# Kernel tuning notes

Hardware: AMD Instinct MI355X
Metric: run time of the kernel (lower is better)

## Reference

```python
import jax, jax.numpy as jnp
import numpy as np

N1, N2, N3 = 40000, 30000, 30000
N = N1 + N2 + N3          # total nodes after vstack
E = 800000                # edges
D_IN = 256                # in_channels
D_HID = 256               # 2 * out_channels
D_OUT = 128               # out_channels


def _glorot(k, shape):
    lim = (6.0 / (shape[0] + shape[1])) ** 0.5
    return jax.random.uniform(k, shape, jnp.float32, -lim, lim)


def setup_inputs() -> dict:
    key = jax.random.key(0)
    ks = jax.random.split(key, 12)
    x1 = jax.random.normal(ks[0], (N1, 128), jnp.float32)
    x2 = jax.random.normal(ks[1], (N2, 256), jnp.float32)
    x3 = jax.random.normal(ks[2], (N3, 64), jnp.float32)
    edge_index = jax.random.randint(ks[3], (2, E), 0, N, jnp.int64)
    return {
        "x1": x1, "x2": x2, "x3": x3,
        "Wp1": _glorot(ks[4], (128, D_IN)), "bp1": jnp.zeros((D_IN,), jnp.float32),
        "Wp2": _glorot(ks[5], (256, D_IN)), "bp2": jnp.zeros((D_IN,), jnp.float32),
        "Wp3": _glorot(ks[6], (64, D_IN)),  "bp3": jnp.zeros((D_IN,), jnp.float32),
        "W1": _glorot(ks[7], (D_IN, D_HID)), "b1": jnp.zeros((D_HID,), jnp.float32),
        "W2": _glorot(ks[8], (D_HID, D_OUT)), "b2": jnp.zeros((D_OUT,), jnp.float32),
        "edge_index": edge_index,
    }


def _gcn_conv(x, W, b, src, dst, dis):
    # PyG GCNConv: h = xW; out[j] = sum_i norm_ij * h[i] (incl. self-loop) + b
    h = x @ W                                   # [N, d_out]
    msg = h[src] * (dis[src] * dis[dst])[:, None]   # [E, d_out] edge messages
    agg = jax.ops.segment_sum(msg, dst, num_segments=N)
    agg = agg + h * (dis * dis)[:, None]        # self-loop term (norm = 1/deg)
    return agg + b


def reference(x1, x2, x3, Wp1, bp1, Wp2, bp2, Wp3, bp3, W1, b1, W2, b2, edge_index):
    # per-type projection + vstack
    x = jnp.concatenate([x1 @ Wp1 + bp1, x2 @ Wp2 + bp2, x3 @ Wp3 + bp3], axis=0)
    # dropout(p=0.5) is identity in eval mode (deterministic baseline)
    src, dst = edge_index[0], edge_index[1]
    # degree with self-loops (in-degree at dst, as in PyG gcn_norm)
    deg = jnp.ones((N,), x.dtype).at[dst].add(1.0)
    dis = jax.lax.rsqrt(deg)                    # deg^{-1/2}
    h = jax.nn.relu(_gcn_conv(x, W1, b1, src, dst, dis))
    return _gcn_conv(h, W2, b2, src, dst, dis)
```

## Files before the change

kernel.cpp:

```cpp
#include <hip/hip_runtime.h>
#include <cstddef>

#define NT 100000
#define NN1 40000
#define NN2 30000
#define NN3 30000
#define EE 800000
#define DIN 256
#define DHID 256
#define DOUT 128

typedef _Float16 f16;
typedef f16 f16x8 __attribute__((ext_vector_type(8)));
typedef f16 f16x4 __attribute__((ext_vector_type(4)));
typedef f16 f16x2 __attribute__((ext_vector_type(2)));
typedef float f32x4 __attribute__((ext_vector_type(4)));

static inline int cdiv(int a, int b) { return (a + b - 1) / b; }

__device__ __forceinline__ void gload_lds16(const f16* g, f16* l) {
    __builtin_amdgcn_global_load_lds(
        (const __attribute__((address_space(1))) void*)g,
        (__attribute__((address_space(3))) void*)l, 16, 0, 0);
}

__global__ void k_hist(const int* __restrict__ dst, int* __restrict__ cnt, int e) {
    int i = blockIdx.x * blockDim.x + threadIdx.x;
    if (i < e) atomicAdd(&cnt[dst[i]], 1);
}

__global__ void k_scan1(const int* __restrict__ cnt, int* __restrict__ rowptr,
                        int* __restrict__ part, float* __restrict__ dis, int n) {
    __shared__ int sums[256];
    int b = blockIdx.x, t = threadIdx.x;
    int base = b * 1024 + t * 4;
    int v0 = (base + 0 < n) ? cnt[base + 0] : 0;
    int v1 = (base + 1 < n) ? cnt[base + 1] : 0;
    int v2 = (base + 2 < n) ? cnt[base + 2] : 0;
    int v3 = (base + 3 < n) ? cnt[base + 3] : 0;
    if (base + 0 < n) dis[base + 0] = rsqrtf((float)v0 + 1.0f);
    if (base + 1 < n) dis[base + 1] = rsqrtf((float)v1 + 1.0f);
    if (base + 2 < n) dis[base + 2] = rsqrtf((float)v2 + 1.0f);
    if (base + 3 < n) dis[base + 3] = rsqrtf((float)v3 + 1.0f);
    int tsum = v0 + v1 + v2 + v3;
    sums[t] = tsum;
    __syncthreads();
    for (int off = 1; off < 256; off <<= 1) {
        int y = (t >= off) ? sums[t - off] : 0;
        __syncthreads();
        sums[t] += y;
        __syncthreads();
    }
    int excl = sums[t] - tsum;
    if (base + 0 < n) rowptr[base + 0] = excl;
    if (base + 1 < n) rowptr[base + 1] = excl + v0;
    if (base + 2 < n) rowptr[base + 2] = excl + v0 + v1;
    if (base + 3 < n) rowptr[base + 3] = excl + v0 + v1 + v2;
    if (t == 255) part[b] = sums[255];
}

__global__ void k_scan2(int* __restrict__ part, int nb) {
    __shared__ int sums[256];
    int t = threadIdx.x;
    int v = (t < nb) ? part[t] : 0;
    sums[t] = v;
    __syncthreads();
    for (int off = 1; off < 256; off <<= 1) {
        int y = (t >= off) ? sums[t - off] : 0;
        __syncthreads();
        sums[t] += y;
        __syncthreads();
    }
    if (t < nb) part[t] = sums[t] - v;
}

__global__ void k_scan3(int* __restrict__ rowptr, const int* __restrict__ part,
                        int n, int total) {
    int i = blockIdx.x * blockDim.x + threadIdx.x;
    if (i < n) rowptr[i] += part[i >> 10];
    if (i == 0) rowptr[n] = total;
}

__global__ void k_fill(const int* __restrict__ src, const int* __restrict__ dst,
                       const int* __restrict__ rowptr, int* __restrict__ cursor,
                       int* __restrict__ e_src, int e) {
    int i = blockIdx.x * blockDim.x + threadIdx.x;
    if (i >= e) return;
    int t = dst[i];
    int pos = atomicAdd(&cursor[t], 1);
    e_src[rowptr[t] + pos] = src[i];
}

__global__ void k_cvt_all(const float* __restrict__ a, int na4,
                          const float* __restrict__ b, int nb4,
                          const float* __restrict__ c, int nc4,
                          f16* __restrict__ o) {
    int i = blockIdx.x * blockDim.x + threadIdx.x;
    const float* s; int j;
    if (i < na4) { s = a; j = i; }
    else if (i < na4 + nb4) { s = b; j = i - na4; }
    else if (i < na4 + nb4 + nc4) { s = c; j = i - na4 - nb4; }
    else return;
    float4 v = reinterpret_cast<const float4*>(s)[j];
    f16x4 r = {(f16)v.x, (f16)v.y, (f16)v.z, (f16)v.w};
    reinterpret_cast<f16x4*>(o)[i] = r;
}

struct TArgs {
    const float *W0, *W1, *W2, *W3, *W4;
    f16 *T0, *T1, *T2, *T3, *T4;
};
__global__ void k_transpose_all(TArgs t) {
    int i = blockIdx.x * blockDim.x + threadIdx.x;
    const float* W; f16* T; int K, N, j;
    if      (i <  32768) { W = t.W0; T = t.T0; K = 128; N = 256; j = i; }
    else if (i <  98304) { W = t.W1; T = t.T1; K = 256; N = 256; j = i - 32768; }
    else if (i < 114688) { W = t.W2; T = t.T2; K =  64; N = 256; j = i - 98304; }
    else if (i < 180224) { W = t.W3; T = t.T3; K = 256; N = 256; j = i - 114688; }
    else if (i < 212992) { W = t.W4; T = t.T4; K = 256; N = 128; j = i - 180224; }
    else return;
    int k = j / N, n = j - k * N;
    T[n * K + k] = (f16)W[j];
}

template<bool RELU_OUT, bool HAS_BIAS>
__global__ __launch_bounds__(256)
void k_hgemm(const f16* __restrict__ A, const f16* __restrict__ BT,
             const float* __restrict__ bias, f16* __restrict__ C,
             int M, int K, int N) {
    __shared__ f16 As[2][4096];
    __shared__ f16 Bs[2][4096];
    const int tid = threadIdx.x;
    const int lane = tid & 63;
    const int wid = tid >> 6;
    const int wm = wid & 1, wn = wid >> 1;
    const int bm = blockIdx.x * 128;
    const int bn = blockIdx.y * 128;
    const int r15 = lane & 15, g = lane >> 4;
    const int sr  = lane >> 2;
    const int chs = (lane & 3) ^ ((lane >> 3) & 3);

    auto stage = [&](int buf, int k0) {
        #pragma unroll
        for (int q = 0; q < 2; ++q) {
            int chunk = wid + q * 4;
            int row = chunk * 16 + sr;
            int ga = bm + row; if (ga >= M) ga = M - 1;
            gload_lds16(A  + (size_t)ga * K + k0 + chs * 8, &As[buf][chunk * 512]);
            gload_lds16(BT + (size_t)(bn + row) * K + k0 + chs * 8, &Bs[buf][chunk * 512]);
        }
    };

    f32x4 acc[4][4] = {};
    const int nsteps = K >> 5;
    stage(0, 0);
    __syncthreads();
    int cur = 0;
    for (int step = 0; step < nsteps; ++step) {
        if (step + 1 < nsteps) stage(cur ^ 1, (step + 1) << 5);
        f16x8 af[4], bf[4];
        const int sl = (g ^ ((r15 >> 1) & 3)) * 8;
        #pragma unroll
        for (int mf = 0; mf < 4; ++mf) {
            int row = wm * 64 + mf * 16 + r15;
            af[mf] = *reinterpret_cast<const f16x8*>(&As[cur][row * 32 + sl]);
        }
        #pragma unroll
        for (int nf = 0; nf < 4; ++nf) {
            int row = wn * 64 + nf * 16 + r15;
            bf[nf] = *reinterpret_cast<const f16x8*>(&Bs[cur][row * 32 + sl]);
        }
        #pragma unroll
        for (int mf = 0; mf < 4; ++mf)
            #pragma unroll
            for (int nf = 0; nf < 4; ++nf)
                acc[mf][nf] = __builtin_amdgcn_mfma_f32_16x16x32_f16(af[mf], bf[nf], acc[mf][nf], 0, 0, 0);
        __syncthreads();
        cur ^= 1;
    }

    #pragma unroll
    for (int mf = 0; mf < 4; ++mf) {
        #pragma unroll
        for (int nf = 0; nf < 4; ++nf) {
            int col = bn + wn * 64 + nf * 16 + r15;
            float bv = HAS_BIAS ? bias[col] : 0.f;
            #pragma unroll
            for (int r = 0; r < 4; ++r) {
                int rowg = bm + wm * 64 + mf * 16 + g * 4 + r;
                if (rowg < M) {
                    float v = acc[mf][nf][r] + bv;
                    if (RELU_OUT) v = fmaxf(v, 0.f);
                    C[(size_t)rowg * N + col] = (f16)v;
                }
            }
        }
    }
}

__global__ void k_gather256(const f16* __restrict__ f, const float* __restrict__ dis,
                            const int* __restrict__ rowptr, const int* __restrict__ e_src,
                            f16* __restrict__ outb, int n) {
    int wid = (int)(((long long)blockIdx.x * blockDim.x + threadIdx.x) >> 6);
    int lane = threadIdx.x & 63;
    if (wid >= n) return;
    float dj = dis[wid];
    int r0 = rowptr[wid], r1 = rowptr[wid + 1];
    int deg = r1 - r0;
    int si = 0; float wi = 0.f;
    if (lane < deg) { si = e_src[r0 + lane]; wi = dis[si]; }
    f16x4 a = reinterpret_cast<const f16x4*>(f + (size_t)wid * 256)[lane];
    float ws = dj * dj;
    float ax = (float)a[0] * ws, ay = (float)a[1] * ws, az = (float)a[2] * ws, aw = (float)a[3] * ws;
    int n64 = deg < 64 ? deg : 64;
    int e = 0;
    for (; e + 4 <= n64; e += 4) {
        int s0 = __shfl(si, e + 0), s1 = __shfl(si, e + 1);
        int s2 = __shfl(si, e + 2), s3 = __shfl(si, e + 3);
        float w0 = __shfl(wi, e + 0) * dj, w1 = __shfl(wi, e + 1) * dj;
        float w2 = __shfl(wi, e + 2) * dj, w3 = __shfl(wi, e + 3) * dj;
        f16x4 u0 = reinterpret_cast<const f16x4*>(f + (size_t)s0 * 256)[lane];
        f16x4 u1 = reinterpret_cast<const f16x4*>(f + (size_t)s1 * 256)[lane];
        f16x4 u2 = reinterpret_cast<const f16x4*>(f + (size_t)s2 * 256)[lane];
        f16x4 u3 = reinterpret_cast<const f16x4*>(f + (size_t)s3 * 256)[lane];
        ax += (float)u0[0] * w0 + (float)u1[0] * w1 + (float)u2[0] * w2 + (float)u3[0] * w3;
        ay += (float)u0[1] * w0 + (float)u1[1] * w1 + (float)u2[1] * w2 + (float)u3[1] * w3;
        az += (float)u0[2] * w0 + (float)u1[2] * w1 + (float)u2[2] * w2 + (float)u3[2] * w3;
        aw += (float)u0[3] * w0 + (float)u1[3] * w1 + (float)u2[3] * w2 + (float)u3[3] * w3;
    }
    for (; e < n64; ++e) {
        int s0 = __shfl(si, e); float w0 = __shfl(wi, e) * dj;
        f16x4 u0 = reinterpret_cast<const f16x4*>(f + (size_t)s0 * 256)[lane];
        ax += (float)u0[0] * w0; ay += (float)u0[1] * w0;
        az += (float)u0[2] * w0; aw += (float)u0[3] * w0;
    }
    for (int e2 = r0 + 64; e2 < r1; ++e2) {
        int s0 = __builtin_amdgcn_readfirstlane(e_src[e2]);
        float w0 = dis[s0] * dj;
        f16x4 u0 = reinterpret_cast<const f16x4*>(f + (size_t)s0 * 256)[lane];
        ax += (float)u0[0] * w0; ay += (float)u0[1] * w0;
        az += (float)u0[2] * w0; aw += (float)u0[3] * w0;
    }
    f16x4 r = {(f16)ax, (f16)ay, (f16)az, (f16)aw};
    reinterpret_cast<f16x4*>(outb + (size_t)wid * 256)[lane] = r;
}

__global__ void k_gather128(const f16* __restrict__ f, const float* __restrict__ dis,
                            const int* __restrict__ rowptr, const int* __restrict__ e_src,
                            const float* __restrict__ bias, float* __restrict__ outb, int n) {
    int wid = (int)(((long long)blockIdx.x * blockDim.x + threadIdx.x) >> 6);
    int lane = threadIdx.x & 63;
    if (wid >= n) return;
    float dj = dis[wid];
    int r0 = rowptr[wid], r1 = rowptr[wid + 1];
    int deg = r1 - r0;
    int si = 0; float wi = 0.f;
    if (lane < deg) { si = e_src[r0 + lane]; wi = dis[si]; }
    f16x2 a = reinterpret_cast<const f16x2*>(f + (size_t)wid * 128)[lane];
    float ws = dj * dj;
    float ax = (float)a[0] * ws, ay = (float)a[1] * ws;
    int n64 = deg < 64 ? deg : 64;
    int e = 0;
    for (; e + 4 <= n64; e += 4) {
        int s0 = __shfl(si, e + 0), s1 = __shfl(si, e + 1);
        int s2 = __shfl(si, e + 2), s3 = __shfl(si, e + 3);
        float w0 = __shfl(wi, e + 0) * dj, w1 = __shfl(wi, e + 1) * dj;
        float w2 = __shfl(wi, e + 2) * dj, w3 = __shfl(wi, e + 3) * dj;
        f16x2 u0 = reinterpret_cast<const f16x2*>(f + (size_t)s0 * 128)[lane];
        f16x2 u1 = reinterpret_cast<const f16x2*>(f + (size_t)s1 * 128)[lane];
        f16x2 u2 = reinterpret_cast<const f16x2*>(f + (size_t)s2 * 128)[lane];
        f16x2 u3 = reinterpret_cast<const f16x2*>(f + (size_t)s3 * 128)[lane];
        ax += (float)u0[0] * w0 + (float)u1[0] * w1 + (float)u2[0] * w2 + (float)u3[0] * w3;
        ay += (float)u0[1] * w0 + (float)u1[1] * w1 + (float)u2[1] * w2 + (float)u3[1] * w3;
    }
    for (; e < n64; ++e) {
        int s0 = __shfl(si, e); float w0 = __shfl(wi, e) * dj;
        f16x2 u0 = reinterpret_cast<const f16x2*>(f + (size_t)s0 * 128)[lane];
        ax += (float)u0[0] * w0; ay += (float)u0[1] * w0;
    }
    for (int e2 = r0 + 64; e2 < r1; ++e2) {
        int s0 = __builtin_amdgcn_readfirstlane(e_src[e2]);
        float w0 = dis[s0] * dj;
        f16x2 u0 = reinterpret_cast<const f16x2*>(f + (size_t)s0 * 128)[lane];
        ax += (float)u0[0] * w0; ay += (float)u0[1] * w0;
    }
    float2 bb = reinterpret_cast<const float2*>(bias)[lane];
    reinterpret_cast<float2*>(outb + (size_t)wid * 128)[lane] = make_float2(ax + bb.x, ay + bb.y);
}

extern "C" void kernel_launch(void* const* d_in, const int* in_sizes, int n_in,
                              void* d_out, int out_size, void* d_ws, size_t ws_size,
                              hipStream_t stream) {
    const float* x1  = (const float*)d_in[0];
    const float* x2  = (const float*)d_in[1];
    const float* x3  = (const float*)d_in[2];
    const float* Wp1 = (const float*)d_in[3];
    const float* bp1 = (const float*)d_in[4];
    const float* Wp2 = (const float*)d_in[5];
    const float* bp2 = (const float*)d_in[6];
    const float* Wp3 = (const float*)d_in[7];
    const float* bp3 = (const float*)d_in[8];
    const float* W1  = (const float*)d_in[9];
    const float* b1  = (const float*)d_in[10];
    const float* W2  = (const float*)d_in[11];
    const float* b2  = (const float*)d_in[12];
    const int*   ei  = (const int*)d_in[13];
    const int* src = ei;
    const int* dst = ei + EE;
    float* out = (float*)d_out;

    char* ws = (char*)d_ws;
    size_t off = 0;
    auto alloc = [&](size_t bytes) {
        char* p = ws + off;
        off += (bytes + 511) & ~(size_t)511;
        return p;
    };
    float* dis    = (float*)alloc((size_t)NT * 4);
    int*   cnt    = (int*)alloc((size_t)NT * 4);
    int*   cursor = (int*)alloc((size_t)NT * 4);
    int*   rowptr = (int*)alloc((size_t)(NT + 1) * 4);
    int*   part   = (int*)alloc(256 * 4);
    int*   e_src  = (int*)alloc((size_t)EE * 4);
    f16*   slotX  = (f16*)alloc((size_t)NT * 256 * 2);
    f16*   slotY  = (f16*)alloc((size_t)NT * 256 * 2);
    f16*   xc     = (f16*)alloc((size_t)(NN1 * 128 + NN2 * 256 + NN3 * 64) * 2);
    f16*   Wp1T   = (f16*)alloc((size_t)256 * 128 * 2);
    f16*   Wp2T   = (f16*)alloc((size_t)256 * 256 * 2);
    f16*   Wp3T   = (f16*)alloc((size_t)256 * 64 * 2);
    f16*   W1T    = (f16*)alloc((size_t)256 * 256 * 2);
    f16*   W2T    = (f16*)alloc((size_t)128 * 256 * 2);

    f16* x1c = xc;
    f16* x2c = xc + (size_t)NN1 * 128;
    f16* x3c = xc + (size_t)NN1 * 128 + (size_t)NN2 * 256;
    f16* x16   = slotX;
    f16* agg16 = slotY;
    f16* h16   = slotX;
    f16* hw216 = slotY;

    const int nb = cdiv(NT, 1024);

    size_t zspan = (size_t)((char*)rowptr - (char*)cnt);
    hipMemsetAsync(cnt, 0, zspan, stream);
    k_hist<<<cdiv(EE, 256), 256, 0, stream>>>(dst, cnt, EE);
    k_scan1<<<nb, 256, 0, stream>>>(cnt, rowptr, part, dis, NT);
    k_scan2<<<1, 256, 0, stream>>>(part, nb);
    k_scan3<<<cdiv(NT, 256), 256, 0, stream>>>(rowptr, part, NT, EE);
    k_fill<<<cdiv(EE, 256), 256, 0, stream>>>(src, dst, rowptr, cursor, e_src, EE);

    {
        int na4 = NN1 * 128 / 4, nb4 = NN2 * 256 / 4, nc4 = NN3 * 64 / 4;
        k_cvt_all<<<cdiv(na4 + nb4 + nc4, 256), 256, 0, stream>>>(x1, na4, x2, nb4, x3, nc4, xc);
        TArgs t = {Wp1, Wp2, Wp3, W1, W2, Wp1T, Wp2T, Wp3T, W1T, W2T};
        k_transpose_all<<<cdiv(212992, 256), 256, 0, stream>>>(t);
    }

    {
        dim3 g1(cdiv(NN1, 128), 2);
        k_hgemm<false, true><<<g1, 256, 0, stream>>>(x1c, Wp1T, bp1, x16, NN1, 128, 256);
        dim3 g2(cdiv(NN2, 128), 2);
        k_hgemm<false, true><<<g2, 256, 0, stream>>>(x2c, Wp2T, bp2, x16 + (size_t)NN1 * 256, NN2, 256, 256);
        dim3 g3(cdiv(NN3, 128), 2);
        k_hgemm<false, true><<<g3, 256, 0, stream>>>(x3c, Wp3T, bp3, x16 + (size_t)(NN1 + NN2) * 256, NN3, 64, 256);
    }

    k_gather256<<<cdiv(NT * 64, 256), 256, 0, stream>>>(x16, dis, rowptr, e_src, agg16, NT);

    {
        dim3 g(cdiv(NT, 128), 2);
        k_hgemm<true, true><<<g, 256, 0, stream>>>(agg16, W1T, b1, h16, NT, 256, 256);
    }

    {
        dim3 g(cdiv(NT, 128), 1);
        k_hgemm<false, false><<<g, 256, 0, stream>>>(h16, W2T, nullptr, hw216, NT, 256, 128);
    }

    k_gather128<<<cdiv(NT * 64, 256), 256, 0, stream>>>(hw216, dis, rowptr, e_src, b2, out, NT);
}
```

Measured before the change: 331.2 us.

## Precompute edge weights in CSR, half-wave gathers, fuse three projection GEMMs

The CSR fill now stores (src, dis[src]*dis[dst]) pairs, so the gather kernels no longer do a dependent dis[] lookup per edge. The gathers move from one wave per node to 32 lanes per node with wider 16-byte vector loads. The three per-type projection GEMMs are merged into one launch using dynamic shared memory. In exchange, the edge array doubles in size and each lane holds more accumulators.

```diff
diff --git a/kernel.cpp b/kernel.cpp
--- a/kernel.cpp
+++ b/kernel.cpp
@@ -13,7 +13,6 @@
 typedef _Float16 f16;
 typedef f16 f16x8 __attribute__((ext_vector_type(8)));
 typedef f16 f16x4 __attribute__((ext_vector_type(4)));
-typedef f16 f16x2 __attribute__((ext_vector_type(2)));
 typedef float f32x4 __attribute__((ext_vector_type(4)));
 
 static inline int cdiv(int a, int b) { return (a + b - 1) / b; }
@@ -82,13 +81,16 @@
 }
 
 __global__ void k_fill(const int* __restrict__ src, const int* __restrict__ dst,
-                       const int* __restrict__ rowptr, int* __restrict__ cursor,
-                       int* __restrict__ e_src, int e) {
+                       const float* __restrict__ dis, const int* __restrict__ rowptr,
+                       int* __restrict__ cursor, int2* __restrict__ e_pairs, int e) {
     int i = blockIdx.x * blockDim.x + threadIdx.x;
     if (i >= e) return;
-    int t = dst[i];
+    int s = src[i], t = dst[i];
     int pos = atomicAdd(&cursor[t], 1);
-    e_src[rowptr[t] + pos] = src[i];
+    int2 p;
+    p.x = s;
+    p.y = __float_as_int(dis[s] * dis[t]);
+    e_pairs[rowptr[t] + pos] = p;
 }
 
 __global__ void k_cvt_all(const float* __restrict__ a, int na4,
@@ -124,18 +126,17 @@
 }
 
 template<bool RELU_OUT, bool HAS_BIAS>
-__global__ __launch_bounds__(256)
-void k_hgemm(const f16* __restrict__ A, const f16* __restrict__ BT,
-             const float* __restrict__ bias, f16* __restrict__ C,
-             int M, int K, int N) {
-    __shared__ f16 As[2][4096];
-    __shared__ f16 Bs[2][4096];
+__device__ __forceinline__
+void hgemm_body(f16* As, f16* Bs,
+                const f16* __restrict__ A, const f16* __restrict__ BT,
+                const float* __restrict__ bias, f16* __restrict__ C,
+                int M, int K, int N, int bx, int by) {
     const int tid = threadIdx.x;
     const int lane = tid & 63;
     const int wid = tid >> 6;
     const int wm = wid & 1, wn = wid >> 1;
-    const int bm = blockIdx.x * 128;
-    const int bn = blockIdx.y * 128;
+    const int bm = bx * 128;
+    const int bn = by * 128;
     const int r15 = lane & 15, g = lane >> 4;
     const int sr  = lane >> 2;
     const int chs = (lane & 3) ^ ((lane >> 3) & 3);
@@ -146,8 +147,8 @@
             int chunk = wid + q * 4;
             int row = chunk * 16 + sr;
             int ga = bm + row; if (ga >= M) ga = M - 1;
-            gload_lds16(A  + (size_t)ga * K + k0 + chs * 8, &As[buf][chunk * 512]);
-            gload_lds16(BT + (size_t)(bn + row) * K + k0 + chs * 8, &Bs[buf][chunk * 512]);
+            gload_lds16(A  + (size_t)ga * K + k0 + chs * 8, As + buf * 4096 + chunk * 512);
+            gload_lds16(BT + (size_t)(bn + row) * K + k0 + chs * 8, Bs + buf * 4096 + chunk * 512);
         }
     };
 
@@ -163,12 +164,12 @@
         #pragma unroll
         for (int mf = 0; mf < 4; ++mf) {
             int row = wm * 64 + mf * 16 + r15;
-            af[mf] = *reinterpret_cast<const f16x8*>(&As[cur][row * 32 + sl]);
+            af[mf] = *reinterpret_cast<const f16x8*>(As + cur * 4096 + row * 32 + sl);
         }
         #pragma unroll
         for (int nf = 0; nf < 4; ++nf) {
             int row = wn * 64 + nf * 16 + r15;
-            bf[nf] = *reinterpret_cast<const f16x8*>(&Bs[cur][row * 32 + sl]);
+            bf[nf] = *reinterpret_cast<const f16x8*>(Bs + cur * 4096 + row * 32 + sl);
         }
         #pragma unroll
         for (int mf = 0; mf < 4; ++mf)
@@ -198,94 +199,132 @@
     }
 }
 
+template<bool RELU_OUT, bool HAS_BIAS>
+__global__ __launch_bounds__(256)
+void k_hgemm(const f16* __restrict__ A, const f16* __restrict__ BT,
+             const float* __restrict__ bias, f16* __restrict__ C,
+             int M, int K, int N) {
+    extern __shared__ f16 smem[];
+    hgemm_body<RELU_OUT, HAS_BIAS>(smem, smem + 8192, A, BT, bias, C, M, K, N,
+                                   blockIdx.x, blockIdx.y);
+}
+
+struct P3 {
+    const f16 *a1, *a2, *a3, *t1, *t2, *t3;
+    const float *b1, *b2, *b3;
+    f16 *o1, *o2, *o3;
+    int g1, g2;
+};
+__global__ __launch_bounds__(256) void k_proj3(P3 p) {
+    extern __shared__ f16 smem[];
+    int bx = blockIdx.x, by = blockIdx.y;
+    if (bx < p.g1)
+        hgemm_body<false, true>(smem, smem + 8192, p.a1, p.t1, p.b1, p.o1, NN1, 128, 256, bx, by);
+    else if (bx < p.g1 + p.g2)
+        hgemm_body<false, true>(smem, smem + 8192, p.a2, p.t2, p.b2, p.o2, NN2, 256, 256, bx - p.g1, by);
+    else
+        hgemm_body<false, true>(smem, smem + 8192, p.a3, p.t3, p.b3, p.o3, NN3, 64, 256, bx - p.g1 - p.g2, by);
+}
+
 __global__ void k_gather256(const f16* __restrict__ f, const float* __restrict__ dis,
-                            const int* __restrict__ rowptr, const int* __restrict__ e_src,
+                            const int* __restrict__ rowptr, const int2* __restrict__ e_pairs,
                             f16* __restrict__ outb, int n) {
-    int wid = (int)(((long long)blockIdx.x * blockDim.x + threadIdx.x) >> 6);
-    int lane = threadIdx.x & 63;
-    if (wid >= n) return;
-    float dj = dis[wid];
-    int r0 = rowptr[wid], r1 = rowptr[wid + 1];
+    int node = (int)(((long long)blockIdx.x * blockDim.x + threadIdx.x) >> 5);
+    int l = threadIdx.x & 31;
+    if (node >= n) return;
+    float dj = dis[node];
+    int r0 = rowptr[node], r1 = rowptr[node + 1];
     int deg = r1 - r0;
     int si = 0; float wi = 0.f;
-    if (lane < deg) { si = e_src[r0 + lane]; wi = dis[si]; }
-    f16x4 a = reinterpret_cast<const f16x4*>(f + (size_t)wid * 256)[lane];
+    if (l < deg) { int2 p = e_pairs[r0 + l]; si = p.x; wi = __int_as_float(p.y); }
+    f16x8 a = reinterpret_cast<const f16x8*>(f + (size_t)node * 256)[l];
     float ws = dj * dj;
-    float ax = (float)a[0] * ws, ay = (float)a[1] * ws, az = (float)a[2] * ws, aw = (float)a[3] * ws;
-    int n64 = deg < 64 ? deg : 64;
+    float acc[8];
+    #pragma unroll
+    for (int k = 0; k < 8; ++k) acc[k] = (float)a[k] * ws;
+    int n32 = deg < 32 ? deg : 32;
     int e = 0;
-    for (; e + 4 <= n64; e += 4) {
-        int s0 = __shfl(si, e + 0), s1 = __shfl(si, e + 1);
-        int s2 = __shfl(si, e + 2), s3 = __shfl(si, e + 3);
-        float w0 = __shfl(wi, e + 0) * dj, w1 = __shfl(wi, e + 1) * dj;
-        float w2 = __shfl(wi, e + 2) * dj, w3 = __shfl(wi, e + 3) * dj;
-        f16x4 u0 = reinterpret_cast<const f16x4*>(f + (size_t)s0 * 256)[lane];
-        f16x4 u1 = reinterpret_cast<const f16x4*>(f + (size_t)s1 * 256)[lane];
-        f16x4 u2 = reinterpret_cast<const f16x4*>(f + (size_t)s2 * 256)[lane];
-        f16x4 u3 = reinterpret_cast<const f16x4*>(f + (size_t)s3 * 256)[lane];
-        ax += (float)u0[0] * w0 + (float)u1[0] * w1 + (float)u2[0] * w2 + (float)u3[0] * w3;
-        ay += (float)u0[1] * w0 + (float)u1[1] * w1 + (float)u2[1] * w2 + (float)u3[1] * w3;
-        az += (float)u0[2] * w0 + (float)u1[2] * w1 + (float)u2[2] * w2 + (float)u3[2] * w3;
-        aw += (float)u0[3] * w0 + (float)u1[3] * w1 + (float)u2[3] * w2 + (float)u3[3] * w3;
-    }
-    for (; e < n64; ++e) {
-        int s0 = __shfl(si, e); float w0 = __shfl(wi, e) * dj;
-        f16x4 u0 = reinterpret_cast<const f16x4*>(f + (size_t)s0 * 256)[lane];
-        ax += (float)u0[0] * w0; ay += (float)u0[1] * w0;
-        az += (float)u0[2] * w0; aw += (float)u0[3] * w0;
-    }
-    for (int e2 = r0 + 64; e2 < r1; ++e2) {
-        int s0 = __builtin_amdgcn_readfirstlane(e_src[e2]);
-        float w0 = dis[s0] * dj;
-        f16x4 u0 = reinterpret_cast<const f16x4*>(f + (size_t)s0 * 256)[lane];
-        ax += (float)u0[0] * w0; ay += (float)u0[1] * w0;
-        az += (float)u0[2] * w0; aw += (float)u0[3] * w0;
-    }
-    f16x4 r = {(f16)ax, (f16)ay, (f16)az, (f16)aw};
-    reinterpret_cast<f16x4*>(outb + (size_t)wid * 256)[lane] = r;
+    for (; e + 4 <= n32; e += 4) {
+        int s0 = __shfl(si, e + 0, 32), s1 = __shfl(si, e + 1, 32);
+        int s2 = __shfl(si, e + 2, 32), s3 = __shfl(si, e + 3, 32);
+        float w0 = __shfl(wi, e + 0, 32), w1 = __shfl(wi, e + 1, 32);
+        float w2 = __shfl(wi, e + 2, 32), w3 = __shfl(wi, e + 3, 32);
+        f16x8 u0 = reinterpret_cast<const f16x8*>(f + (size_t)s0 * 256)[l];
+        f16x8 u1 = reinterpret_cast<const f16x8*>(f + (size_t)s1 * 256)[l];
+        f16x8 u2 = reinterpret_cast<const f16x8*>(f + (size_t)s2 * 256)[l];
+        f16x8 u3 = reinterpret_cast<const f16x8*>(f + (size_t)s3 * 256)[l];
+        #pragma unroll
+        for (int k = 0; k < 8; ++k)
+            acc[k] += (float)u0[k] * w0 + (float)u1[k] * w1 + (float)u2[k] * w2 + (float)u3[k] * w3;
+    }
+    for (; e < n32; ++e) {
+        int s0 = __shfl(si, e, 32);
+        float w0 = __shfl(wi, e, 32);
+        f16x8 u0 = reinterpret_cast<const f16x8*>(f + (size_t)s0 * 256)[l];
+        #pragma unroll
+        for (int k = 0; k < 8; ++k) acc[k] += (float)u0[k] * w0;
+    }
+    for (int e2 = r0 + 32; e2 < r1; ++e2) {
+        int2 p = e_pairs[e2];
+        float w0 = __int_as_float(p.y);
+        f16x8 u0 = reinterpret_cast<const f16x8*>(f + (size_t)p.x * 256)[l];
+        #pragma unroll
+        for (int k = 0; k < 8; ++k) acc[k] += (float)u0[k] * w0;
+    }
+    f16x8 r;
+    #pragma unroll
+    for (int k = 0; k < 8; ++k) r[k] = (f16)acc[k];
+    reinterpret_cast<f16x8*>(outb + (size_t)node * 256)[l] = r;
 }
 
 __global__ void k_gather128(const f16* __restrict__ f, const float* __restrict__ dis,
-                            const int* __restrict__ rowptr, const int* __restrict__ e_src,
+                            const int* __restrict__ rowptr, const int2* __restrict__ e_pairs,
                             const float* __restrict__ bias, float* __restrict__ outb, int n) {
-    int wid = (int)(((long long)blockIdx.x * blockDim.x + threadIdx.x) >> 6);
-    int lane = threadIdx.x & 63;
-    if (wid >= n) return;
-    float dj = dis[wid];
-    int r0 = rowptr[wid], r1 = rowptr[wid + 1];
+    int node = (int)(((long long)blockIdx.x * blockDim.x + threadIdx.x) >> 5);
+    int l = threadIdx.x & 31;
+    if (node >= n) return;
+    float dj = dis[node];
+    int r0 = rowptr[node], r1 = rowptr[node + 1];
     int deg = r1 - r0;
     int si = 0; float wi = 0.f;
-    if (lane < deg) { si = e_src[r0 + lane]; wi = dis[si]; }
-    f16x2 a = reinterpret_cast<const f16x2*>(f + (size_t)wid * 128)[lane];
+    if (l < deg) { int2 p = e_pairs[r0 + l]; si = p.x; wi = __int_as_float(p.y); }
+    f16x4 a = reinterpret_cast<const f16x4*>(f + (size_t)node * 128)[l];
     float ws = dj * dj;
-    float ax = (float)a[0] * ws, ay = (float)a[1] * ws;
-    int n64 = deg < 64 ? deg : 64;
+    float acc[4];
+    #pragma unroll
+    for (int k = 0; k < 4; ++k) acc[k] = (float)a[k] * ws;
+    int n32 = deg < 32 ? deg : 32;
     int e = 0;
-    for (; e + 4 <= n64; e += 4) {
-        int s0 = __shfl(si, e + 0), s1 = __shfl(si, e + 1);
-        int s2 = __shfl(si, e + 2), s3 = __shfl(si, e + 3);
-        float w0 = __shfl(wi, e + 0) * dj, w1 = __shfl(wi, e + 1) * dj;
-        float w2 = __shfl(wi, e + 2) * dj, w3 = __shfl(wi, e + 3) * dj;
-        f16x2 u0 = reinterpret_cast<const f16x2*>(f + (size_t)s0 * 128)[lane];
-        f16x2 u1 = reinterpret_cast<const f16x2*>(f + (size_t)s1 * 128)[lane];
-        f16x2 u2 = reinterpret_cast<const f16x2*>(f + (size_t)s2 * 128)[lane];
-        f16x2 u3 = reinterpret_cast<const f16x2*>(f + (size_t)s3 * 128)[lane];
-        ax += (float)u0[0] * w0 + (float)u1[0] * w1 + (float)u2[0] * w2 + (float)u3[0] * w3;
-        ay += (float)u0[1] * w0 + (float)u1[1] * w1 + (float)u2[1] * w2 + (float)u3[1] * w3;
-    }
-    for (; e < n64; ++e) {
-        int s0 = __shfl(si, e); float w0 = __shfl(wi, e) * dj;
-        f16x2 u0 = reinterpret_cast<const f16x2*>(f + (size_t)s0 * 128)[lane];
-        ax += (float)u0[0] * w0; ay += (float)u0[1] * w0;
-    }
-    for (int e2 = r0 + 64; e2 < r1; ++e2) {
-        int s0 = __builtin_amdgcn_readfirstlane(e_src[e2]);
-        float w0 = dis[s0] * dj;
-        f16x2 u0 = reinterpret_cast<const f16x2*>(f + (size_t)s0 * 128)[lane];
-        ax += (float)u0[0] * w0; ay += (float)u0[1] * w0;
-    }
-    float2 bb = reinterpret_cast<const float2*>(bias)[lane];
-    reinterpret_cast<float2*>(outb + (size_t)wid * 128)[lane] = make_float2(ax + bb.x, ay + bb.y);
+    for (; e + 4 <= n32; e += 4) {
+        int s0 = __shfl(si, e + 0, 32), s1 = __shfl(si, e + 1, 32);
+        int s2 = __shfl(si, e + 2, 32), s3 = __shfl(si, e + 3, 32);
+        float w0 = __shfl(wi, e + 0, 32), w1 = __shfl(wi, e + 1, 32);
+        float w2 = __shfl(wi, e + 2, 32), w3 = __shfl(wi, e + 3, 32);
+        f16x4 u0 = reinterpret_cast<const f16x4*>(f + (size_t)s0 * 128)[l];
+        f16x4 u1 = reinterpret_cast<const f16x4*>(f + (size_t)s1 * 128)[l];
+        f16x4 u2 = reinterpret_cast<const f16x4*>(f + (size_t)s2 * 128)[l];
+        f16x4 u3 = reinterpret_cast<const f16x4*>(f + (size_t)s3 * 128)[l];
+        #pragma unroll
+        for (int k = 0; k < 4; ++k)
+            acc[k] += (float)u0[k] * w0 + (float)u1[k] * w1 + (float)u2[k] * w2 + (float)u3[k] * w3;
+    }
+    for (; e < n32; ++e) {
+        int s0 = __shfl(si, e, 32);
+        float w0 = __shfl(wi, e, 32);
+        f16x4 u0 = reinterpret_cast<const f16x4*>(f + (size_t)s0 * 128)[l];
+        #pragma unroll
+        for (int k = 0; k < 4; ++k) acc[k] += (float)u0[k] * w0;
+    }
+    for (int e2 = r0 + 32; e2 < r1; ++e2) {
+        int2 p = e_pairs[e2];
+        float w0 = __int_as_float(p.y);
+        f16x4 u0 = reinterpret_cast<const f16x4*>(f + (size_t)p.x * 128)[l];
+        #pragma unroll
+        for (int k = 0; k < 4; ++k) acc[k] += (float)u0[k] * w0;
+    }
+    float4 bb = reinterpret_cast<const float4*>(bias)[l];
+    float4 r = make_float4(acc[0] + bb.x, acc[1] + bb.y, acc[2] + bb.z, acc[3] + bb.w);
+    reinterpret_cast<float4*>(outb + (size_t)node * 128)[l] = r;
 }
 
 extern "C" void kernel_launch(void* const* d_in, const int* in_sizes, int n_in,
@@ -321,7 +360,7 @@
     int*   cursor = (int*)alloc((size_t)NT * 4);
     int*   rowptr = (int*)alloc((size_t)(NT + 1) * 4);
     int*   part   = (int*)alloc(256 * 4);
-    int*   e_src  = (int*)alloc((size_t)EE * 4);
+    int2*  e_pairs= (int2*)alloc((size_t)EE * 8);
     f16*   slotX  = (f16*)alloc((size_t)NT * 256 * 2);
     f16*   slotY  = (f16*)alloc((size_t)NT * 256 * 2);
     f16*   xc     = (f16*)alloc((size_t)(NN1 * 128 + NN2 * 256 + NN3 * 64) * 2);
@@ -347,7 +386,7 @@
     k_scan1<<<nb, 256, 0, stream>>>(cnt, rowptr, part, dis, NT);
     k_scan2<<<1, 256, 0, stream>>>(part, nb);
     k_scan3<<<cdiv(NT, 256), 256, 0, stream>>>(rowptr, part, NT, EE);
-    k_fill<<<cdiv(EE, 256), 256, 0, stream>>>(src, dst, rowptr, cursor, e_src, EE);
+    k_fill<<<cdiv(EE, 256), 256, 0, stream>>>(src, dst, dis, rowptr, cursor, e_pairs, EE);
 
     {
         int na4 = NN1 * 128 / 4, nb4 = NN2 * 256 / 4, nc4 = NN3 * 64 / 4;
@@ -357,25 +396,24 @@
     }
 
     {
-        dim3 g1(cdiv(NN1, 128), 2);
-        k_hgemm<false, true><<<g1, 256, 0, stream>>>(x1c, Wp1T, bp1, x16, NN1, 128, 256);
-        dim3 g2(cdiv(NN2, 128), 2);
-        k_hgemm<false, true><<<g2, 256, 0, stream>>>(x2c, Wp2T, bp2, x16 + (size_t)NN1 * 256, NN2, 256, 256);
-        dim3 g3(cdiv(NN3, 128), 2);
-        k_hgemm<false, true><<<g3, 256, 0, stream>>>(x3c, Wp3T, bp3, x16 + (size_t)(NN1 + NN2) * 256, NN3, 64, 256);
-    }
-
-    k_gather256<<<cdiv(NT * 64, 256), 256, 0, stream>>>(x16, dis, rowptr, e_src, agg16, NT);
+        P3 p = {x1c, x2c, x3c, Wp1T, Wp2T, Wp3T, bp1, bp2, bp3,
+                x16, x16 + (size_t)NN1 * 256, x16 + (size_t)(NN1 + NN2) * 256,
+                cdiv(NN1, 128), cdiv(NN2, 128)};
+        dim3 g(cdiv(NN1, 128) + cdiv(NN2, 128) + cdiv(NN3, 128), 2);
+        k_proj3<<<g, 256, 32768, stream>>>(p);
+    }
+
+    k_gather256<<<cdiv(NT * 32, 256), 256, 0, stream>>>(x16, dis, rowptr, e_pairs, agg16, NT);
 
     {
         dim3 g(cdiv(NT, 128), 2);
-        k_hgemm<true, true><<<g, 256, 0, stream>>>(agg16, W1T, b1, h16, NT, 256, 256);
+        k_hgemm<true, true><<<g, 256, 32768, stream>>>(agg16, W1T, b1, h16, NT, 256, 256);
     }
 
     {
         dim3 g(cdiv(NT, 128), 1);
-        k_hgemm<false, false><<<g, 256, 0, stream>>>(h16, W2T, nullptr, hw216, NT, 256, 128);
-    }
-
-    k_gather128<<<cdiv(NT * 64, 256), 256, 0, stream>>>(hw216, dis, rowptr, e_src, b2, out, NT);
-}
+        k_hgemm<false, false><<<g, 256, 32768, stream>>>(h16, W2T, nullptr, hw216, NT, 256, 128);
+    }
+
+    k_gather128<<<cdiv(NT * 32, 256), 256, 0, stream>>>(hw216, dis, rowptr, e_pairs, b2, out, NT);
+}
```

Measured after the change: 313.4 us. 1.06x faster.
